# Optimization experiments

Hardware: AMD Instinct MI355X
Metric: run time of the kernel (lower is better)

The kernel has to match this reference:

```python
import jax, jax.numpy as jnp
import numpy as np

P, H_OUT, D, NX = 32, 1, 256, 16
S_A = -0.1

def layernorm(x, g, b, eps=1e-5):
    mu = jnp.mean(x, axis=-1, keepdims=True)
    var = jnp.var(x, axis=-1, keepdims=True)
    return (x - mu) * jax.lax.rsqrt(var + eps) * g + b

def setup_inputs() -> dict:
    key = jax.random.key(0)
    ks = jax.random.split(key, 16)
    B, L = 8, 2048
    y = jax.random.normal(ks[0], (B, L, P), jnp.float32)
    Win = jax.random.normal(ks[1], (P, D), jnp.float32) / np.sqrt(P)
    bin_ = jnp.zeros((D,), jnp.float32)
    ng = jnp.ones((D,), jnp.float32); nb = jnp.zeros((D,), jnp.float32)
    # A = -10*rand + s_A, with A[:,0] = s_A (fix first state of each channel)
    A = -10.0 * jax.random.uniform(ks[2], (D, NX), jnp.float32) + S_A
    A = A.at[:, 0].set(S_A)
    W_B = jax.random.normal(ks[3], (NX, D), jnp.float32)
    W_C = jax.random.normal(ks[4], (NX, D), jnp.float32)
    q_delta = jax.random.normal(ks[5], (D,), jnp.float32)
    p_delta = jax.random.normal(ks[6], (1,), jnp.float32)
    nfg = jnp.ones((D,), jnp.float32); nfb = jnp.zeros((D,), jnp.float32)
    W1 = jax.random.normal(ks[7], (D, D), jnp.float32) / np.sqrt(D)
    b1 = jnp.zeros((D,), jnp.float32)
    W2 = jax.random.normal(ks[8], (D, H_OUT * P), jnp.float32) / np.sqrt(D)
    b2 = jnp.zeros((H_OUT * P,), jnp.float32)
    return {"y": y, "Win": Win, "bin_": bin_, "ng": ng, "nb": nb, "A": A,
            "W_B": W_B, "W_C": W_C, "q_delta": q_delta, "p_delta": p_delta,
            "nfg": nfg, "nfb": nfb, "W1": W1, "b1": b1, "W2": W2, "b2": b2}

def selective_scan(u, delta, A, Bm, Cm):
    # u: (B,L,D), delta: (B,L), A: (D,NX), Bm/Cm: (B,L,NX)
    dA = jnp.exp(delta[..., None, None] * A)                      # (B,L,D,NX)
    dBu = delta[..., None, None] * Bm[:, :, None, :] * u[..., None]  # (B,L,D,NX)
    x0 = jnp.zeros((u.shape[0], u.shape[2], A.shape[1]), u.dtype)
    def step(x, inp):
        dA_t, dBu_t, C_t = inp
        x = dA_t * x + dBu_t                                      # (B,D,NX)
        y_t = jnp.einsum('bdn,bn->bd', x, C_t)
        return x, y_t
    _, ys = jax.lax.scan(step, x0, (dA.transpose(1, 0, 2, 3),
                                    dBu.transpose(1, 0, 2, 3),
                                    Cm.transpose(1, 0, 2)))
    return ys.transpose(1, 0, 2)                                  # (B,L,D)

def reference(y, Win, bin_, ng, nb, A, W_B, W_C, q_delta, p_delta,
              nfg, nfb, W1, b1, W2, b2):
    B, L, _ = y.shape
    h = y @ Win + bin_                                            # (B,L,D)
    hn = layernorm(h, ng, nb)
    delta = jax.nn.softplus(p_delta[0] + jnp.einsum('bld,d->bl', hn, q_delta))
    Bm = jnp.einsum('nd,bld->bln', W_B, hn)
    Cm = jnp.einsum('nd,bld->bln', W_C, hn)
    upd = selective_scan(hn, delta, A, Bm, Cm)
    h = h + upd
    h = layernorm(h, nfg, nfb)
    out = jax.nn.gelu(h @ W1 + b1, approximate=False) @ W2 + b2
    return out.reshape(B, L, H_OUT, P)
```

## Files before the change

### kernel.cpp

```cpp
#include <hip/hip_runtime.h>
#include <math.h>

#define D 256
#define NX 16
#define L 2048
#define NBATCH 8
#define NTOK (NBATCH * L)
#define CL 32
#define NCH (L / CL)
#define LOG2E 1.44269504088896340736f

typedef float f32x4 __attribute__((ext_vector_type(4)));
typedef short bf16x8 __attribute__((ext_vector_type(8)));

__device__ __forceinline__ unsigned short f2bf(float x) {
  unsigned u = __float_as_uint(x);
  u = u + 0x7fffu + ((u >> 16) & 1u);
  return (unsigned short)(u >> 16);
}
__device__ __forceinline__ float bf2f(unsigned short h) {
  return __uint_as_float(((unsigned)h) << 16);
}

__global__ __launch_bounds__(256) void k0_prep(const float* __restrict__ A,
                                               const float* __restrict__ WB,
                                               const float* __restrict__ WC,
                                               const float* __restrict__ Win,
                                               const float* __restrict__ W1,
                                               const float* __restrict__ W2,
                                               const float* __restrict__ nfg,
                                               const float* __restrict__ nfb,
                                               float* __restrict__ At,
                                               unsigned short* __restrict__ W1fh,
                                               unsigned short* __restrict__ W1fl,
                                               unsigned short* __restrict__ W2fh,
                                               unsigned short* __restrict__ W2fl,
                                               unsigned short* __restrict__ Winfh,
                                               unsigned short* __restrict__ Winfl,
                                               unsigned short* __restrict__ Wbcfh,
                                               unsigned short* __restrict__ Wbcfl,
                                               float* __restrict__ u1,
                                               float* __restrict__ v1) {
  int i = blockIdx.x * 256 + threadIdx.x;
  if (i < 4096) {
    int d = i >> 4, n = i & 15;
    At[n * D + d] = A[i] * LOG2E;
  } else if (i < 12288) {
    int e = i - 4096;
    int j = e & 7, l = (e >> 3) & 63, tt = e >> 9;
    int k = ((l >> 4) << 3) + j;
    int n = tt * 16 + (l & 15);
    float x = Win[k * 256 + n];
    unsigned short h = f2bf(x);
    Winfh[e] = h;
    Winfl[e] = f2bf(x - bf2f(h));
  } else if (i < 20480) {
    int e = i - 12288;
    int j = e & 7, l = (e >> 3) & 63, q = e >> 9;
    int s = q >> 1, tt = q & 1;
    int k = s * 32 + ((l >> 4) << 3) + j;
    int n = tt * 16 + (l & 15);
    float x = (n < 16) ? WB[n * 256 + k] : WC[(n - 16) * 256 + k];
    unsigned short h = f2bf(x);
    Wbcfh[e] = h;
    Wbcfl[e] = f2bf(x - bf2f(h));
  } else if (i < 86016) {
    int e = i - 20480;
    int j = e & 7, l = (e >> 3) & 63, tt = (e >> 9) & 15, s = e >> 13;
    int k = s * 32 + ((l >> 4) << 3) + j;
    int n = tt * 16 + (l & 15);
    float x = W1[k * 256 + n] * nfg[k];
    unsigned short h = f2bf(x);
    W1fh[e] = h;
    W1fl[e] = f2bf(x - bf2f(h));
  } else if (i < 94208) {
    int e = i - 86016;
    int j = e & 7, l = (e >> 3) & 63, tt = (e >> 9) & 1, s = e >> 10;
    int k = s * 32 + ((l >> 4) << 3) + j;
    int n = tt * 16 + (l & 15);
    float x = W2[k * 32 + n];
    unsigned short h = f2bf(x);
    W2fh[e] = h;
    W2fl[e] = f2bf(x - bf2f(h));
  } else if (i < 94464) {
    int c = i - 94208;
    float s = 0.f;
    for (int d = 0; d < 256; ++d) s += nfg[d] * W1[d * 256 + c];
    u1[c] = s;
  } else if (i < 94720) {
    int c = i - 94464;
    float s = 0.f;
    for (int d = 0; d < 256; ++d) s += nfb[d] * W1[d * 256 + c];
    v1[c] = s;
  }
}

__global__ __launch_bounds__(512, 4) void k1a_front_scan(
    const float* __restrict__ y, const float* __restrict__ bin_,
    const float* __restrict__ ng, const float* __restrict__ nb,
    const float* __restrict__ qd, const float* __restrict__ pd,
    const float* __restrict__ At,
    const unsigned short* __restrict__ Winfh,
    const unsigned short* __restrict__ Winfl,
    const unsigned short* __restrict__ Wbcfh,
    const unsigned short* __restrict__ Wbcfl,
    float* __restrict__ hn, float* __restrict__ delta,
    float* __restrict__ Bm, float* __restrict__ Cm,
    float* __restrict__ muv, float* __restrict__ irsv,
    float* __restrict__ EX, float* __restrict__ T) {
  __shared__ float sy[32][36];
  __shared__ float sh[32][260];
  __shared__ float sB[32][NX];
  __shared__ float sred[32][16];
  __shared__ float sdelta[32];
  __shared__ float smu[32];
  __shared__ float srstd[32];
  __shared__ __align__(16) unsigned short sChA_h[32 * 256];
  __shared__ __align__(16) unsigned short sChA_l[32 * 256];
  int t = threadIdx.x;
  int l = t & 63;
  int w = t >> 6;
  int tok0 = blockIdx.x * 32;
  if (t < 256) {
    int row = t >> 3, c4 = t & 7;
    *(float4*)&sy[row][c4 * 4] = ((const float4*)(y + (size_t)tok0 * 32))[t];
  }
  __syncthreads();
  f32x4 acc[2][2];
  {
    bf16x8 yah[2], yal[2];
    int k0 = (l >> 4) << 3;
    #pragma unroll
    for (int m = 0; m < 2; ++m) {
      int row = m * 16 + (l & 15);
      float4 f0 = *(float4*)&sy[row][k0];
      float4 f1 = *(float4*)&sy[row][k0 + 4];
      float v0 = f0.x, v1_ = f0.y, v2 = f0.z, v3 = f0.w;
      float v4 = f1.x, v5 = f1.y, v6 = f1.z, v7 = f1.w;
      unsigned short h0 = f2bf(v0), h1 = f2bf(v1_), h2 = f2bf(v2), h3 = f2bf(v3);
      unsigned short h4 = f2bf(v4), h5 = f2bf(v5), h6 = f2bf(v6), h7 = f2bf(v7);
      yah[m][0] = (short)h0; yah[m][1] = (short)h1; yah[m][2] = (short)h2; yah[m][3] = (short)h3;
      yah[m][4] = (short)h4; yah[m][5] = (short)h5; yah[m][6] = (short)h6; yah[m][7] = (short)h7;
      yal[m][0] = (short)f2bf(v0 - bf2f(h0)); yal[m][1] = (short)f2bf(v1_ - bf2f(h1));
      yal[m][2] = (short)f2bf(v2 - bf2f(h2)); yal[m][3] = (short)f2bf(v3 - bf2f(h3));
      yal[m][4] = (short)f2bf(v4 - bf2f(h4)); yal[m][5] = (short)f2bf(v5 - bf2f(h5));
      yal[m][6] = (short)f2bf(v6 - bf2f(h6)); yal[m][7] = (short)f2bf(v7 - bf2f(h7));
    }
    const bf16x8* Bh = (const bf16x8*)Winfh;
    const bf16x8* Bl = (const bf16x8*)Winfl;
    #pragma unroll
    for (int n = 0; n < 2; ++n) {
      int tt = w * 2 + n;
      bf16x8 bh = Bh[tt * 64 + l];
      bf16x8 bl = Bl[tt * 64 + l];
      #pragma unroll
      for (int m = 0; m < 2; ++m) {
        f32x4 a = {0.f, 0.f, 0.f, 0.f};
        a = __builtin_amdgcn_mfma_f32_16x16x32_bf16(yah[m], bh, a, 0, 0, 0);
        a = __builtin_amdgcn_mfma_f32_16x16x32_bf16(yal[m], bh, a, 0, 0, 0);
        a = __builtin_amdgcn_mfma_f32_16x16x32_bf16(yah[m], bl, a, 0, 0, 0);
        a = __builtin_amdgcn_mfma_f32_16x16x32_bf16(yal[m], bl, a, 0, 0, 0);
        acc[m][n] = a;
      }
    }
  }
  int c0 = w * 32 + (l & 15), c1 = c0 + 16;
  {
    float b0 = bin_[c0], b1v = bin_[c1];
    #pragma unroll
    for (int m = 0; m < 2; ++m)
      #pragma unroll
      for (int r = 0; r < 4; ++r) { acc[m][0][r] += b0; acc[m][1][r] += b1v; }
  }
  {
    #pragma unroll
    for (int m = 0; m < 2; ++m)
      #pragma unroll
      for (int r = 0; r < 4; ++r) {
        float a0 = acc[m][0][r], a1 = acc[m][1][r];
        float s1 = a0 + a1;
        float s2 = a0 * a0 + a1 * a1;
        #pragma unroll
        for (int off = 1; off < 16; off <<= 1) {
          s1 += __shfl_xor(s1, off);
          s2 += __shfl_xor(s2, off);
        }
        if ((l & 15) == 0) {
          int tok = m * 16 + ((l >> 4) << 2) + r;
          sred[tok][w * 2] = s1;
          sred[tok][w * 2 + 1] = s2;
        }
      }
  }
  __syncthreads();
  if (t < 32) {
    float s1 = 0.f, s2 = 0.f;
    #pragma unroll
    for (int q = 0; q < 8; ++q) { s1 += sred[t][q * 2]; s2 += sred[t][q * 2 + 1]; }
    float mu = s1 * (1.f / D);
    float var = s2 * (1.f / D) - mu * mu;
    float rstd = rsqrtf(var + 1e-5f);
    smu[t] = mu;
    srstd[t] = rstd;
    muv[tok0 + t] = mu;
    irsv[tok0 + t] = sqrtf(var + 1e-5f);
  }
  __syncthreads();
  {
    float g0 = ng[c0], g1 = ng[c1];
    float nb0 = nb[c0], nb1 = nb[c1];
    float q0 = qd[c0], q1 = qd[c1];
    float ddv[2][4];
    #pragma unroll
    for (int m = 0; m < 2; ++m)
      #pragma unroll
      for (int r = 0; r < 4; ++r) {
        int tok = m * 16 + ((l >> 4) << 2) + r;
        float mu = smu[tok], rstd = srstd[tok];
        float h0 = (acc[m][0][r] - mu) * rstd * g0 + nb0;
        float h1 = (acc[m][1][r] - mu) * rstd * g1 + nb1;
        sh[tok][c0] = h0;
        sh[tok][c1] = h1;
        float dx = h0 * q0 + h1 * q1;
        #pragma unroll
        for (int off = 1; off < 16; off <<= 1) dx += __shfl_xor(dx, off);
        ddv[m][r] = dx;
      }
    if ((l & 15) == 0) {
      #pragma unroll
      for (int m = 0; m < 2; ++m)
        #pragma unroll
        for (int r = 0; r < 4; ++r)
          sred[m * 16 + ((l >> 4) << 2) + r][w] = ddv[m][r];
    }
  }
  __syncthreads();
  if (t < 32) {
    float dsum = 0.f;
    #pragma unroll
    for (int q = 0; q < 8; ++q) dsum += sred[t][q];
    float xx = pd[0] + dsum;
    float dv = (xx > 20.f) ? xx : log1pf(expf(xx));
    delta[tok0 + t] = dv;
    sdelta[t] = dv;
    float tv = dv;
    #pragma unroll
    for (int off = 1; off < 32; off <<= 1) tv += __shfl_xor(tv, off);
    if (t == 0) T[blockIdx.x] = tv;
  }
  {
    int row = t & 31;
    int cq = (t >> 5) * 16;
    float4 f0 = *(float4*)&sh[row][cq];
    float4 f1 = *(float4*)&sh[row][cq + 4];
    float4 f2 = *(float4*)&sh[row][cq + 8];
    float4 f3 = *(float4*)&sh[row][cq + 12];
    float vv[16] = {f0.x, f0.y, f0.z, f0.w, f1.x, f1.y, f1.z, f1.w,
                    f2.x, f2.y, f2.z, f2.w, f3.x, f3.y, f3.z, f3.w};
    unsigned hw[8], lw[8];
    #pragma unroll
    for (int p = 0; p < 8; ++p) {
      unsigned short ha = f2bf(vv[2 * p]), hb = f2bf(vv[2 * p + 1]);
      unsigned short la = f2bf(vv[2 * p] - bf2f(ha));
      unsigned short lb = f2bf(vv[2 * p + 1] - bf2f(hb));
      hw[p] = (unsigned)ha | ((unsigned)hb << 16);
      lw[p] = (unsigned)la | ((unsigned)lb << 16);
    }
    unsigned base = (unsigned)row * 512;
    #pragma unroll
    for (int g = 0; g < 2; ++g) {
      unsigned off = ((unsigned)(cq * 2 + g * 16)) ^ ((unsigned)(row & 7) << 4);
      uint4 hv4 = {hw[g * 4], hw[g * 4 + 1], hw[g * 4 + 2], hw[g * 4 + 3]};
      uint4 lv4 = {lw[g * 4], lw[g * 4 + 1], lw[g * 4 + 2], lw[g * 4 + 3]};
      *(uint4*)((char*)sChA_h + base + off) = hv4;
      *(uint4*)((char*)sChA_l + base + off) = lv4;
    }
  }
  __syncthreads();
  if (w < 4) {
    int mw = w & 1, nw = w >> 1;
    int row = mw * 16 + (l & 15);
    unsigned abase = (unsigned)row * 512;
    const bf16x8* B2h = (const bf16x8*)Wbcfh;
    const bf16x8* B2l = (const bf16x8*)Wbcfl;
    f32x4 acc2 = {0.f, 0.f, 0.f, 0.f};
    #pragma unroll
    for (int s = 0; s < 8; ++s) {
      unsigned off = ((unsigned)(s * 64 + ((l >> 4) << 4))) ^ ((unsigned)(row & 7) << 4);
      bf16x8 ah = *(const bf16x8*)((const char*)sChA_h + abase + off);
      bf16x8 al = *(const bf16x8*)((const char*)sChA_l + abase + off);
      int bi = (s * 2 + nw) * 64 + l;
      bf16x8 bh = B2h[bi];
      bf16x8 bl = B2l[bi];
      acc2 = __builtin_amdgcn_mfma_f32_16x16x32_bf16(ah, bh, acc2, 0, 0, 0);
      acc2 = __builtin_amdgcn_mfma_f32_16x16x32_bf16(al, bh, acc2, 0, 0, 0);
      acc2 = __builtin_amdgcn_mfma_f32_16x16x32_bf16(ah, bl, acc2, 0, 0, 0);
      acc2 = __builtin_amdgcn_mfma_f32_16x16x32_bf16(al, bl, acc2, 0, 0, 0);
    }
    int tokr = mw * 16 + ((l >> 4) << 2);
    int colc = l & 15;
    if (nw == 0) {
      #pragma unroll
      for (int r = 0; r < 4; ++r) {
        Bm[(size_t)(tok0 + tokr + r) * NX + colc] = acc2[r];
        sB[tokr + r][colc] = acc2[r];
      }
    } else {
      #pragma unroll
      for (int r = 0; r < 4; ++r)
        Cm[(size_t)(tok0 + tokr + r) * NX + colc] = acc2[r];
    }
  } else {
    float4* dst = (float4*)(hn + (size_t)tok0 * D);
    for (int i = t - 256; i < 2048; i += 256) {
      int row = i >> 6, c4 = i & 63;
      dst[i] = *(float4*)&sh[row][c4 * 4];
    }
  }
  __syncthreads();
  {
    int half = t >> 8;
    int d = t & 255;
    float a8[8], x8[8];
    #pragma unroll
    for (int n = 0; n < 8; ++n) {
      a8[n] = At[(half * 8 + n) * D + d];
      x8[n] = 0.f;
    }
    for (int lo = 0; lo < CL; ++lo) {
      float dlt = sdelta[lo];
      float du = dlt * sh[lo][d];
      #pragma unroll
      for (int n = 0; n < 8; ++n)
        x8[n] = fmaf(exp2f(dlt * a8[n]), x8[n], du * sB[lo][half * 8 + n]);
    }
    size_t exbase = (size_t)blockIdx.x * (NX * D) + d;
    #pragma unroll
    for (int n = 0; n < 8; ++n) EX[exbase + (half * 8 + n) * D] = x8[n];
  }
}

__global__ __launch_bounds__(64) void k2b_chunkscan(
    const float* __restrict__ At, const float* __restrict__ T,
    float* __restrict__ EX) {
  __shared__ float sT[NCH];
  int b = blockIdx.x >> 6;
  int rem = ((blockIdx.x & 63) << 6) | threadIdx.x;
  sT[threadIdx.x] = T[b * NCH + threadIdx.x];
  __syncthreads();
  float A2 = At[rem];
  size_t base = ((size_t)b << 18) + rem;
  float eq[8];
  #pragma unroll
  for (int j = 0; j < 8; ++j) eq[j] = EX[base + ((size_t)j << 12)];
  float x = 0.f;
  #pragma unroll 8
  for (int c = 0; c < NCH; ++c) {
    float e = eq[c & 7];
    if (c + 8 < NCH) eq[c & 7] = EX[base + ((size_t)(c + 8) << 12)];
    EX[base + ((size_t)c << 12)] = x;
    x = fmaf(exp2f(sT[c] * A2), x, e);
  }
}

__device__ __forceinline__ float gelu_exact(float x) {
  return 0.5f * x * (1.f + erff(x * 0.70710678118654752440f));
}

__global__ __launch_bounds__(256, 4) void k2cd_scan_mlp(
    const float* __restrict__ hn, const float* __restrict__ delta,
    const float* __restrict__ Bm, const float* __restrict__ Cm,
    const float* __restrict__ At, const float* __restrict__ EX,
    const float* __restrict__ muv, const float* __restrict__ irsv,
    const float* __restrict__ ng, const float* __restrict__ nb,
    const unsigned short* __restrict__ W1fh, const unsigned short* __restrict__ W1fl,
    const unsigned short* __restrict__ W2fh, const unsigned short* __restrict__ W2fl,
    const float* __restrict__ u1, const float* __restrict__ v1,
    const float* __restrict__ b1, const float* __restrict__ b2,
    float* __restrict__ out) {
  __shared__ __align__(16) unsigned short sAh[32 * 256];
  __shared__ __align__(16) unsigned short sAl[32 * 256];
  __shared__ float sB[32][NX];
  __shared__ float sC[32][NX];
  __shared__ float sdelta[32];
  __shared__ float smu1[32];
  __shared__ float sirs1[32];
  __shared__ float sstat[32][8];
  __shared__ float srstd2[32];
  __shared__ float smur2[32];
  int t = threadIdx.x;
  int l = t & 63, w = t >> 6;
  int tok0 = blockIdx.x * 32;
  size_t tokbase = (size_t)tok0;
  if (t < 32) {
    sdelta[t] = delta[tokbase + t];
    smu1[t] = muv[tokbase + t];
    sirs1[t] = irsv[tokbase + t];
  }
  for (int i = t; i < 32 * NX; i += 256) {
    ((float*)sB)[i] = Bm[tokbase * NX + i];
    ((float*)sC)[i] = Cm[tokbase * NX + i];
  }
  float a16[16], x16[16];
  size_t exbase = (size_t)blockIdx.x * (NX * D) + t;
  #pragma unroll
  for (int n = 0; n < 16; ++n) {
    a16[n] = At[n * D + t];
    x16[n] = EX[exbase + n * D];
  }
  float nb_d = nb[t];
  float invg = 1.0f / ng[t];
  __syncthreads();
  for (int lo = 0; lo < CL; ++lo) {
    float hv = hn[(tokbase + lo) * D + t];
    float dlt = sdelta[lo];
    float du = dlt * hv;
    float p = 0.f;
    #pragma unroll
    for (int n = 0; n < 16; ++n) {
      x16[n] = fmaf(exp2f(dlt * a16[n]), x16[n], du * sB[lo][n]);
      p = fmaf(x16[n], sC[lo][n], p);
    }
    float h = fmaf((hv - nb_d) * invg, sirs1[lo], smu1[lo]);
    float v = h + p;
    float s1 = v, s2 = v * v;
    #pragma unroll
    for (int off = 1; off < 64; off <<= 1) {
      s1 += __shfl_xor(s1, off);
      s2 += __shfl_xor(s2, off);
    }
    if (l == 0) { sstat[lo][w * 2] = s1; sstat[lo][w * 2 + 1] = s2; }
    unsigned short vh = f2bf(v);
    unsigned short vl = f2bf(v - bf2f(vh));
    unsigned off16 = ((unsigned)(t * 2)) ^ ((unsigned)((lo & 7) << 4));
    *(unsigned short*)((char*)sAh + lo * 512 + off16) = vh;
    *(unsigned short*)((char*)sAl + lo * 512 + off16) = vl;
  }
  __syncthreads();
  if (t < 32) {
    float s1 = sstat[t][0] + sstat[t][2] + sstat[t][4] + sstat[t][6];
    float s2 = sstat[t][1] + sstat[t][3] + sstat[t][5] + sstat[t][7];
    float mu = s1 * (1.f / D);
    float var = s2 * (1.f / D) - mu * mu;
    float rstd = rsqrtf(var + 1e-5f);
    srstd2[t] = rstd;
    smur2[t] = mu * rstd;
  }
  __syncthreads();
  const bf16x8* B1h = (const bf16x8*)W1fh;
  const bf16x8* B1l = (const bf16x8*)W1fl;
  f32x4 acc[2][4];
  #pragma unroll
  for (int m = 0; m < 2; ++m)
    #pragma unroll
    for (int n = 0; n < 4; ++n) {
      f32x4 z4 = {0.f, 0.f, 0.f, 0.f};
      acc[m][n] = z4;
    }
  #pragma unroll 2
  for (int s = 0; s < 8; ++s) {
    bf16x8 ah[2], al[2];
    #pragma unroll
    for (int m = 0; m < 2; ++m) {
      int row = m * 16 + (l & 15);
      unsigned off16 = ((unsigned)(s * 64 + ((l >> 4) << 4))) ^ ((unsigned)(row & 7) << 4);
      ah[m] = *(const bf16x8*)((const char*)sAh + row * 512 + off16);
      al[m] = *(const bf16x8*)((const char*)sAl + row * 512 + off16);
    }
    #pragma unroll
    for (int n = 0; n < 4; ++n) {
      int bi = (s * 16 + w * 4 + n) * 64 + l;
      bf16x8 bh = B1h[bi];
      bf16x8 bl = B1l[bi];
      #pragma unroll
      for (int m = 0; m < 2; ++m) {
        acc[m][n] = __builtin_amdgcn_mfma_f32_16x16x32_bf16(ah[m], bh, acc[m][n], 0, 0, 0);
        acc[m][n] = __builtin_amdgcn_mfma_f32_16x16x32_bf16(al[m], bh, acc[m][n], 0, 0, 0);
        acc[m][n] = __builtin_amdgcn_mfma_f32_16x16x32_bf16(ah[m], bl, acc[m][n], 0, 0, 0);
        acc[m][n] = __builtin_amdgcn_mfma_f32_16x16x32_bf16(al[m], bl, acc[m][n], 0, 0, 0);
      }
    }
  }
  __syncthreads();
  #pragma unroll
  for (int n = 0; n < 4; ++n) {
    int colz = w * 64 + n * 16 + (l & 15);
    float u1c = u1[colz];
    float v1c = v1[colz] + b1[colz];
    #pragma unroll
    for (int m = 0; m < 2; ++m) {
      #pragma unroll
      for (int r = 0; r < 4; ++r) {
        int row = m * 16 + ((l >> 4) << 2) + r;
        float zpre = acc[m][n][r] * srstd2[row] - smur2[row] * u1c + v1c;
        float zv = gelu_exact(zpre);
        unsigned short zh = f2bf(zv);
        unsigned short zl = f2bf(zv - bf2f(zh));
        unsigned off16 = ((unsigned)(colz * 2)) ^ ((unsigned)(row & 7) << 4);
        *(unsigned short*)((char*)sAh + row * 512 + off16) = zh;
        *(unsigned short*)((char*)sAl + row * 512 + off16) = zl;
      }
    }
  }
  __syncthreads();
  int mw = w >> 1, nw = w & 1;
  const bf16x8* B2h = (const bf16x8*)W2fh;
  const bf16x8* B2l = (const bf16x8*)W2fl;
  f32x4 acc2 = {0.f, 0.f, 0.f, 0.f};
  #pragma unroll 2
  for (int s = 0; s < 8; ++s) {
    int row = mw * 16 + (l & 15);
    unsigned off16 = ((unsigned)(s * 64 + ((l >> 4) << 4))) ^ ((unsigned)(row & 7) << 4);
    bf16x8 zh8 = *(const bf16x8*)((const char*)sAh + row * 512 + off16);
    bf16x8 zl8 = *(const bf16x8*)((const char*)sAl + row * 512 + off16);
    int bi = (s * 2 + nw) * 64 + l;
    bf16x8 bh = B2h[bi];
    bf16x8 bl = B2l[bi];
    acc2 = __builtin_amdgcn_mfma_f32_16x16x32_bf16(zh8, bh, acc2, 0, 0, 0);
    acc2 = __builtin_amdgcn_mfma_f32_16x16x32_bf16(zl8, bh, acc2, 0, 0, 0);
    acc2 = __builtin_amdgcn_mfma_f32_16x16x32_bf16(zh8, bl, acc2, 0, 0, 0);
    acc2 = __builtin_amdgcn_mfma_f32_16x16x32_bf16(zl8, bl, acc2, 0, 0, 0);
  }
  int colo = nw * 16 + (l & 15);
  float b2v = b2[colo];
  #pragma unroll
  for (int r = 0; r < 4; ++r) {
    int row = mw * 16 + ((l >> 4) << 2) + r;
    out[(size_t)(tok0 + row) * 32 + colo] = acc2[r] + b2v;
  }
}

extern "C" void kernel_launch(void* const* d_in, const int* in_sizes, int n_in,
                              void* d_out, int out_size, void* d_ws, size_t ws_size,
                              hipStream_t stream) {
  const float* y    = (const float*)d_in[0];
  const float* Win  = (const float*)d_in[1];
  const float* bin_ = (const float*)d_in[2];
  const float* ng   = (const float*)d_in[3];
  const float* nb   = (const float*)d_in[4];
  const float* A    = (const float*)d_in[5];
  const float* WB   = (const float*)d_in[6];
  const float* WC   = (const float*)d_in[7];
  const float* qd   = (const float*)d_in[8];
  const float* pd   = (const float*)d_in[9];
  const float* nfg  = (const float*)d_in[10];
  const float* nfb  = (const float*)d_in[11];
  const float* W1   = (const float*)d_in[12];
  const float* b1   = (const float*)d_in[13];
  const float* W2   = (const float*)d_in[14];
  const float* b2   = (const float*)d_in[15];

  float* ws = (float*)d_ws;
  float* hnbuf = ws;
  float* delta = ws + 4194304;
  float* Bm    = delta + NTOK;
  float* Cm    = Bm + NTOK * NX;
  float* muv   = Cm + NTOK * NX;
  float* irsv  = muv + NTOK;
  float* Tbuf  = irsv + NTOK;
  float* At    = Tbuf + NBATCH * NCH;
  float* EX    = At + D * NX;
  unsigned short* W1fh  = (unsigned short*)(EX + 2097152);
  unsigned short* W1fl  = W1fh + 65536;
  unsigned short* W2fh  = W1fl + 65536;
  unsigned short* W2fl  = W2fh + 8192;
  unsigned short* Winfh = W2fl + 8192;
  unsigned short* Winfl = Winfh + 8192;
  unsigned short* Wbcfh = Winfl + 8192;
  unsigned short* Wbcfl = Wbcfh + 8192;
  float* u1 = (float*)(Wbcfl + 8192);
  float* v1 = u1 + 256;

  k0_prep<<<370, 256, 0, stream>>>(A, WB, WC, Win, W1, W2, nfg, nfb, At,
                                   W1fh, W1fl, W2fh, W2fl,
                                   Winfh, Winfl, Wbcfh, Wbcfl, u1, v1);
  k1a_front_scan<<<NTOK / 32, 512, 0, stream>>>(y, bin_, ng, nb, qd, pd, At,
                                                Winfh, Winfl, Wbcfh, Wbcfl,
                                                hnbuf, delta, Bm, Cm,
                                                muv, irsv, EX, Tbuf);
  k2b_chunkscan<<<NBATCH * 64, 64, 0, stream>>>(At, Tbuf, EX);
  k2cd_scan_mlp<<<NTOK / 32, 256, 0, stream>>>(hnbuf, delta, Bm, Cm, At, EX,
                                               muv, irsv, ng, nb,
                                               W1fh, W1fl, W2fh, W2fl,
                                               u1, v1, b1, b2, (float*)d_out);
}
```

Measured before the change: 201.0 us.

## Double k2cd block to 512 threads and move layernorm stats after scan

The scan+MLP kernel now launches 512 threads per block. Only the first 256 threads run the per-channel scan. All 8 waves then compute the second layernorm statistics from the bf16 hi/lo values in shared memory, replacing the per-step shuffle reductions inside the scan loop. The W1 GEMM is split across 8 waves with half the accumulators each, while the small W2 GEMM stays on 4 waves. This aims to remove the serial reduction cost from the scan and spread the MFMA work over more waves. The cost is idle waves during the scan, and statistics taken from the split-bf16 reconstruction rather than the exact fp32 values.

```diff
diff --git a/kernel.cpp b/kernel.cpp
--- a/kernel.cpp
+++ b/kernel.cpp
@@ -367,7 +367,7 @@
   return 0.5f * x * (1.f + erff(x * 0.70710678118654752440f));
 }
 
-__global__ __launch_bounds__(256, 4) void k2cd_scan_mlp(
+__global__ __launch_bounds__(512, 4) void k2cd_scan_mlp(
     const float* __restrict__ hn, const float* __restrict__ delta,
     const float* __restrict__ Bm, const float* __restrict__ Cm,
     const float* __restrict__ At, const float* __restrict__ EX,
@@ -385,7 +385,6 @@
   __shared__ float sdelta[32];
   __shared__ float smu1[32];
   __shared__ float sirs1[32];
-  __shared__ float sstat[32][8];
   __shared__ float srstd2[32];
   __shared__ float smur2[32];
   int t = threadIdx.x;
@@ -397,63 +396,77 @@
     smu1[t] = muv[tokbase + t];
     sirs1[t] = irsv[tokbase + t];
   }
-  for (int i = t; i < 32 * NX; i += 256) {
-    ((float*)sB)[i] = Bm[tokbase * NX + i];
-    ((float*)sC)[i] = Cm[tokbase * NX + i];
-  }
+  ((float*)sB)[t] = Bm[tokbase * NX + t];
+  ((float*)sC)[t] = Cm[tokbase * NX + t];
   float a16[16], x16[16];
-  size_t exbase = (size_t)blockIdx.x * (NX * D) + t;
-  #pragma unroll
-  for (int n = 0; n < 16; ++n) {
-    a16[n] = At[n * D + t];
-    x16[n] = EX[exbase + n * D];
-  }
-  float nb_d = nb[t];
-  float invg = 1.0f / ng[t];
-  __syncthreads();
-  for (int lo = 0; lo < CL; ++lo) {
-    float hv = hn[(tokbase + lo) * D + t];
-    float dlt = sdelta[lo];
-    float du = dlt * hv;
-    float p = 0.f;
+  float nb_d = 0.f, invg = 1.f;
+  if (t < 256) {
+    size_t exbase = (size_t)blockIdx.x * (NX * D) + t;
     #pragma unroll
     for (int n = 0; n < 16; ++n) {
-      x16[n] = fmaf(exp2f(dlt * a16[n]), x16[n], du * sB[lo][n]);
-      p = fmaf(x16[n], sC[lo][n], p);
-    }
-    float h = fmaf((hv - nb_d) * invg, sirs1[lo], smu1[lo]);
-    float v = h + p;
-    float s1 = v, s2 = v * v;
-    #pragma unroll
-    for (int off = 1; off < 64; off <<= 1) {
-      s1 += __shfl_xor(s1, off);
-      s2 += __shfl_xor(s2, off);
-    }
-    if (l == 0) { sstat[lo][w * 2] = s1; sstat[lo][w * 2 + 1] = s2; }
-    unsigned short vh = f2bf(v);
-    unsigned short vl = f2bf(v - bf2f(vh));
-    unsigned off16 = ((unsigned)(t * 2)) ^ ((unsigned)((lo & 7) << 4));
-    *(unsigned short*)((char*)sAh + lo * 512 + off16) = vh;
-    *(unsigned short*)((char*)sAl + lo * 512 + off16) = vl;
-  }
-  __syncthreads();
-  if (t < 32) {
-    float s1 = sstat[t][0] + sstat[t][2] + sstat[t][4] + sstat[t][6];
-    float s2 = sstat[t][1] + sstat[t][3] + sstat[t][5] + sstat[t][7];
-    float mu = s1 * (1.f / D);
-    float var = s2 * (1.f / D) - mu * mu;
-    float rstd = rsqrtf(var + 1e-5f);
-    srstd2[t] = rstd;
-    smur2[t] = mu * rstd;
+      a16[n] = At[n * D + t];
+      x16[n] = EX[exbase + n * D];
+    }
+    nb_d = nb[t];
+    invg = 1.0f / ng[t];
+  }
+  __syncthreads();
+  if (t < 256) {
+    for (int lo = 0; lo < CL; ++lo) {
+      float hv = hn[(tokbase + lo) * D + t];
+      float dlt = sdelta[lo];
+      float du = dlt * hv;
+      float p = 0.f;
+      #pragma unroll
+      for (int n = 0; n < 16; ++n) {
+        x16[n] = fmaf(exp2f(dlt * a16[n]), x16[n], du * sB[lo][n]);
+        p = fmaf(x16[n], sC[lo][n], p);
+      }
+      float h = fmaf((hv - nb_d) * invg, sirs1[lo], smu1[lo]);
+      float v = h + p;
+      unsigned short vh = f2bf(v);
+      unsigned short vl = f2bf(v - bf2f(vh));
+      unsigned off16 = ((unsigned)(t * 2)) ^ ((unsigned)((lo & 7) << 4));
+      *(unsigned short*)((char*)sAh + lo * 512 + off16) = vh;
+      *(unsigned short*)((char*)sAl + lo * 512 + off16) = vl;
+    }
+  }
+  __syncthreads();
+  {
+    #pragma unroll
+    for (int p = 0; p < 4; ++p) {
+      int tok = w * 4 + p;
+      unsigned off = ((unsigned)(l * 8)) ^ ((unsigned)((tok & 7) << 4));
+      uint2 hv2 = *(uint2*)((char*)sAh + tok * 512 + off);
+      uint2 lv2 = *(uint2*)((char*)sAl + tok * 512 + off);
+      float v0 = bf2f((unsigned short)(hv2.x & 0xffff)) + bf2f((unsigned short)(lv2.x & 0xffff));
+      float v1_ = bf2f((unsigned short)(hv2.x >> 16)) + bf2f((unsigned short)(lv2.x >> 16));
+      float v2 = bf2f((unsigned short)(hv2.y & 0xffff)) + bf2f((unsigned short)(lv2.y & 0xffff));
+      float v3 = bf2f((unsigned short)(hv2.y >> 16)) + bf2f((unsigned short)(lv2.y >> 16));
+      float s1 = v0 + v1_ + v2 + v3;
+      float s2 = v0 * v0 + v1_ * v1_ + v2 * v2 + v3 * v3;
+      #pragma unroll
+      for (int off2 = 1; off2 < 64; off2 <<= 1) {
+        s1 += __shfl_xor(s1, off2);
+        s2 += __shfl_xor(s2, off2);
+      }
+      if (l == 0) {
+        float mu = s1 * (1.f / D);
+        float var = s2 * (1.f / D) - mu * mu;
+        float rstd = rsqrtf(var + 1e-5f);
+        srstd2[tok] = rstd;
+        smur2[tok] = mu * rstd;
+      }
+    }
   }
   __syncthreads();
   const bf16x8* B1h = (const bf16x8*)W1fh;
   const bf16x8* B1l = (const bf16x8*)W1fl;
-  f32x4 acc[2][4];
+  f32x4 acc[2][2];
   #pragma unroll
   for (int m = 0; m < 2; ++m)
     #pragma unroll
-    for (int n = 0; n < 4; ++n) {
+    for (int n = 0; n < 2; ++n) {
       f32x4 z4 = {0.f, 0.f, 0.f, 0.f};
       acc[m][n] = z4;
     }
@@ -468,8 +481,8 @@
       al[m] = *(const bf16x8*)((const char*)sAl + row * 512 + off16);
     }
     #pragma unroll
-    for (int n = 0; n < 4; ++n) {
-      int bi = (s * 16 + w * 4 + n) * 64 + l;
+    for (int n = 0; n < 2; ++n) {
+      int bi = (s * 16 + w * 2 + n) * 64 + l;
       bf16x8 bh = B1h[bi];
       bf16x8 bl = B1l[bi];
       #pragma unroll
@@ -483,8 +496,8 @@
   }
   __syncthreads();
   #pragma unroll
-  for (int n = 0; n < 4; ++n) {
-    int colz = w * 64 + n * 16 + (l & 15);
+  for (int n = 0; n < 2; ++n) {
+    int colz = w * 32 + n * 16 + (l & 15);
     float u1c = u1[colz];
     float v1c = v1[colz] + b1[colz];
     #pragma unroll
@@ -503,30 +516,32 @@
     }
   }
   __syncthreads();
-  int mw = w >> 1, nw = w & 1;
-  const bf16x8* B2h = (const bf16x8*)W2fh;
-  const bf16x8* B2l = (const bf16x8*)W2fl;
-  f32x4 acc2 = {0.f, 0.f, 0.f, 0.f};
-  #pragma unroll 2
-  for (int s = 0; s < 8; ++s) {
-    int row = mw * 16 + (l & 15);
-    unsigned off16 = ((unsigned)(s * 64 + ((l >> 4) << 4))) ^ ((unsigned)(row & 7) << 4);
-    bf16x8 zh8 = *(const bf16x8*)((const char*)sAh + row * 512 + off16);
-    bf16x8 zl8 = *(const bf16x8*)((const char*)sAl + row * 512 + off16);
-    int bi = (s * 2 + nw) * 64 + l;
-    bf16x8 bh = B2h[bi];
-    bf16x8 bl = B2l[bi];
-    acc2 = __builtin_amdgcn_mfma_f32_16x16x32_bf16(zh8, bh, acc2, 0, 0, 0);
-    acc2 = __builtin_amdgcn_mfma_f32_16x16x32_bf16(zl8, bh, acc2, 0, 0, 0);
-    acc2 = __builtin_amdgcn_mfma_f32_16x16x32_bf16(zh8, bl, acc2, 0, 0, 0);
-    acc2 = __builtin_amdgcn_mfma_f32_16x16x32_bf16(zl8, bl, acc2, 0, 0, 0);
-  }
-  int colo = nw * 16 + (l & 15);
-  float b2v = b2[colo];
-  #pragma unroll
-  for (int r = 0; r < 4; ++r) {
-    int row = mw * 16 + ((l >> 4) << 2) + r;
-    out[(size_t)(tok0 + row) * 32 + colo] = acc2[r] + b2v;
+  if (w < 4) {
+    int mw = w >> 1, nw = w & 1;
+    const bf16x8* B2h = (const bf16x8*)W2fh;
+    const bf16x8* B2l = (const bf16x8*)W2fl;
+    f32x4 acc2 = {0.f, 0.f, 0.f, 0.f};
+    #pragma unroll 2
+    for (int s = 0; s < 8; ++s) {
+      int row = mw * 16 + (l & 15);
+      unsigned off16 = ((unsigned)(s * 64 + ((l >> 4) << 4))) ^ ((unsigned)(row & 7) << 4);
+      bf16x8 zh8 = *(const bf16x8*)((const char*)sAh + row * 512 + off16);
+      bf16x8 zl8 = *(const bf16x8*)((const char*)sAl + row * 512 + off16);
+      int bi = (s * 2 + nw) * 64 + l;
+      bf16x8 bh = B2h[bi];
+      bf16x8 bl = B2l[bi];
+      acc2 = __builtin_amdgcn_mfma_f32_16x16x32_bf16(zh8, bh, acc2, 0, 0, 0);
+      acc2 = __builtin_amdgcn_mfma_f32_16x16x32_bf16(zl8, bh, acc2, 0, 0, 0);
+      acc2 = __builtin_amdgcn_mfma_f32_16x16x32_bf16(zh8, bl, acc2, 0, 0, 0);
+      acc2 = __builtin_amdgcn_mfma_f32_16x16x32_bf16(zl8, bl, acc2, 0, 0, 0);
+    }
+    int colo = nw * 16 + (l & 15);
+    float b2v = b2[colo];
+    #pragma unroll
+    for (int r = 0; r < 4; ++r) {
+      int row = mw * 16 + ((l >> 4) << 2) + r;
+      out[(size_t)(tok0 + row) * 32 + colo] = acc2[r] + b2v;
+    }
   }
 }
 
@@ -579,7 +594,7 @@
                                                 hnbuf, delta, Bm, Cm,
                                                 muv, irsv, EX, Tbuf);
   k2b_chunkscan<<<NBATCH * 64, 64, 0, stream>>>(At, Tbuf, EX);
-  k2cd_scan_mlp<<<NTOK / 32, 256, 0, stream>>>(hnbuf, delta, Bm, Cm, At, EX,
+  k2cd_scan_mlp<<<NTOK / 32, 512, 0, stream>>>(hnbuf, delta, Bm, Cm, At, EX,
                                                muv, irsv, ng, nb,
                                                W1fh, W1fl, W2fh, W2fl,
                                                u1, v1, b1, b2, (float*)d_out);
```

After: 194.0 us. 3.5% less time.
